# Kernel optimization log

Hardware: AMD Instinct MI355X
Metric: run time of the kernel (lower is better)

## Reference

```python
import jax, jax.numpy as jnp
import numpy as np

EMBED = 384; HEADS = 12; POINTS = 9; LAYERS = 2
KFG = 20; KBG = 50; NITER = 10
B = 4; H = 64; W = 64


def _layer_norm(x, g, b, eps=1e-5):
    m = x.mean(-1, keepdims=True)
    v = ((x - m) ** 2).mean(-1, keepdims=True)
    return (x - m) * jax.lax.rsqrt(v + eps) * g + b


def _sine_pos(pad, C):
    # pad [B,H,W], 1.0 = padded. SinePositionalEncoding(num_feats=C//2, normalize=True)
    nf = C // 2
    not_m = 1.0 - pad
    y = jnp.cumsum(not_m, axis=1)
    x = jnp.cumsum(not_m, axis=2)
    eps = 1e-6; sc = 2.0 * np.pi
    y = y / (y[:, -1:, :] + eps) * sc
    x = x / (x[:, :, -1:] + eps) * sc
    t = jnp.arange(nf, dtype=jnp.float32)
    dim_t = 10000.0 ** (2.0 * jnp.floor(t / 2.0) / nf)
    px = x[..., None] / dim_t
    py = y[..., None] / dim_t
    def inter(p):
        b_, h_, w_, _ = p.shape
        return jnp.stack((jnp.sin(p[..., 0::2]), jnp.cos(p[..., 1::2])), -1).reshape(b_, h_, w_, nf)
    pos = jnp.concatenate([inter(py), inter(px)], -1)  # [B,H,W,C]
    return pos.reshape(pad.shape[0], -1, C)


def _kmeans(x, w, K, n_iter):
    # masked Lloyd k-means. x [B,N,C], w [B,N] in {0,1} (1 = member of the group)
    Bq, N, C = x.shape
    score = w - (jnp.arange(N, dtype=x.dtype) / N) * 1e-3  # earliest in-group points first
    _, idx = jax.lax.top_k(score, K)
    centers = jnp.take_along_axis(x, idx[:, :, None], axis=1)  # [B,K,C]
    xsq = jnp.sum(x * x, -1)
    def body(i, c):
        d = xsq[:, :, None] - 2.0 * jnp.einsum('bnc,bkc->bnk', x, c) + jnp.sum(c * c, -1)[:, None, :]
        a = jax.nn.one_hot(jnp.argmin(d, -1), K, dtype=x.dtype) * w[:, :, None]
        num = jnp.einsum('bnk,bnc->bkc', a, x)
        den = jnp.sum(a, 1)[:, :, None]
        return jnp.where(den > 0, num / jnp.maximum(den, 1e-6), c)
    return jax.lax.fori_loop(0, n_iter, body, centers)


def _bilinear(value, loc, Hs, Ws):
    # value [B,heads,HW,hd]; loc [B,N,heads,P,2] normalized (x,y); zero padding outside
    Bq, nh, HW, hd = value.shape
    x = loc[..., 0] * Ws - 0.5
    y = loc[..., 1] * Hs - 0.5
    x0 = jnp.floor(x); y0 = jnp.floor(y)
    def tr(t):
        return jnp.transpose(t, (0, 2, 1, 3)).reshape(Bq, nh, -1)  # -> [B,heads,N*P]
    wx = tr(x - x0)[..., None]
    wy = tr(y - y0)[..., None]
    x0i = x0.astype(jnp.int32); y0i = y0.astype(jnp.int32)
    def gather(xi, yi):
        valid = (xi >= 0) & (xi < Ws) & (yi >= 0) & (yi < Hs)
        idx = jnp.clip(yi, 0, Hs - 1) * Ws + jnp.clip(xi, 0, Ws - 1)
        g = jnp.take_along_axis(value, tr(idx)[..., None], axis=2)  # [B,heads,N*P,hd]
        return g * tr(valid.astype(value.dtype))[..., None]
    v00 = gather(x0i, y0i)
    v01 = gather(x0i + 1, y0i)
    v10 = gather(x0i, y0i + 1)
    v11 = gather(x0i + 1, y0i + 1)
    out = v00 * (1 - wx) * (1 - wy) + v01 * wx * (1 - wy) + v10 * (1 - wx) * wy + v11 * wx * wy
    return out.reshape(Bq, nh, -1, POINTS, hd)  # [B,heads,N,P,hd]


def _forward(s_x, s_padding_mask, supp_mask, Wv, bv, Woff, boff, Wa, ba, Wout, bout,
             ln1_g, ln1_b, Wf1, Wf2, ln2_g, ln2_b):
    Bq, C, Hs, Ws = s_x.shape
    N = Hs * Ws
    hd = C // HEADS
    pad = (s_padding_mask[:, 0] == 255.0).astype(s_x.dtype)  # 1 = padded
    obj = (supp_mask[:, 0] == 1.0).astype(s_x.dtype)
    x = s_x.reshape(Bq, C, N).transpose(0, 2, 1)  # [B,N,C]
    padf = pad.reshape(Bq, N)
    objf = obj.reshape(Bq, N)
    # FG/BG k-means clustering of valid pixels (Cluster tool, n_iter=10)
    fg_c = _kmeans(x, objf * (1.0 - padf), KFG, NITER)
    bg_c = _kmeans(x, (1.0 - objf) * (1.0 - padf), KBG, NITER)
    pos = _sine_pos(pad, C)
    ry, rx = jnp.meshgrid(jnp.linspace(0.5, Hs - 0.5, Hs) / Hs,
                          jnp.linspace(0.5, Ws - 0.5, Ws) / Ws, indexing='ij')
    ref = jnp.stack([rx.reshape(-1), ry.reshape(-1)], -1)[None]  # [1,N,2] (x,y)
    wh = jnp.array([Ws, Hs], dtype=s_x.dtype)
    for l in range(LAYERS):
        q = x + pos
        v = (x * (1.0 - padf)[..., None]) @ Wv[l] + bv[l]
        v = v.reshape(Bq, N, HEADS, hd).transpose(0, 2, 1, 3)  # [B,heads,N,hd]
        off = (q @ Woff[l] + boff[l]).reshape(Bq, N, HEADS, POINTS, 2)
        aw = jax.nn.softmax((q @ Wa[l] + ba[l]).reshape(Bq, N, HEADS, POINTS), axis=-1)
        loc = ref[:, :, None, None, :] + off / wh
        samp = _bilinear(v, loc, Hs, Ws)  # [B,heads,N,P,hd]
        attn = jnp.einsum('bhnpd,bnhp->bnhd', samp, aw).reshape(Bq, N, C)
        x = _layer_norm(x + attn @ Wout[l] + bout[l], ln1_g[l], ln1_b[l])
        x = _layer_norm(x + jax.nn.relu(x @ Wf1[l]) @ Wf2[l], ln2_g[l], ln2_b[l])
    return jnp.concatenate([x, fg_c, bg_c], axis=1)  # [B, N+70, C]


def setup_inputs():
    key = jax.random.key(0)
    ks = jax.random.split(key, 12)
    dt = jnp.float32
    s = 0.02
    p = lambda k, shp: jax.random.normal(k, shp, dt) * s
    s_x = jax.random.normal(ks[0], (B, EMBED, H, W), dt)
    pad = jnp.zeros((B, 1, H, W), dt).at[:, :, :, W - 8:].set(255.0)  # right border padded
    supp_mask = (jax.random.uniform(ks[1], (B, 1, H, W)) < 0.15).astype(dt)
    return dict(
        s_x=s_x, s_padding_mask=pad, supp_mask=supp_mask,
        Wv=p(ks[2], (LAYERS, EMBED, EMBED)), bv=jnp.zeros((LAYERS, EMBED), dt),
        Woff=p(ks[3], (LAYERS, EMBED, HEADS * POINTS * 2)), boff=p(ks[4], (LAYERS, HEADS * POINTS * 2)),
        Wa=p(ks[5], (LAYERS, EMBED, HEADS * POINTS)), ba=jnp.zeros((LAYERS, HEADS * POINTS), dt),
        Wout=p(ks[6], (LAYERS, EMBED, EMBED)), bout=jnp.zeros((LAYERS, EMBED), dt),
        ln1_g=jnp.ones((LAYERS, EMBED), dt), ln1_b=jnp.zeros((LAYERS, EMBED), dt),
        Wf1=p(ks[7], (LAYERS, EMBED, 3 * EMBED)), Wf2=p(ks[8], (LAYERS, 3 * EMBED, EMBED)),
        ln2_g=jnp.ones((LAYERS, EMBED), dt), ln2_b=jnp.zeros((LAYERS, EMBED), dt))


def reference(s_x, s_padding_mask, supp_mask, Wv, bv, Woff, boff, Wa, ba, Wout, bout,
              ln1_g, ln1_b, Wf1, Wf2, ln2_g, ln2_b):
    return _forward(s_x, s_padding_mask, supp_mask, Wv, bv, Woff, boff, Wa, ba, Wout, bout,
                    ln1_g, ln1_b, Wf1, Wf2, ln2_g, ln2_b)
```

## Files before the change

kernel.cpp:

```cpp
#include <hip/hip_runtime.h>
#include <hip/hip_bf16.h>
#include <math.h>

#define NB 4
#define CE 384
#define NH 12
#define DH 32
#define NPTS 9
#define NLAYERS 2
#define KFG 20
#define KBG 50
#define NITER 10
#define HDIM 64
#define WDIM 64
#define NPIX 4096
#define BNTOT (NB * NPIX)
#define NROW (NPIX + KFG + KBG)
#define TWO_PI 6.283185307179586f

#define AS1 __attribute__((address_space(1)))
#define AS3 __attribute__((address_space(3)))

typedef __attribute__((ext_vector_type(8))) short short8;
typedef __attribute__((ext_vector_type(4))) float float4v;

static __device__ __forceinline__ unsigned short f2bf(float f) {
  __hip_bfloat16 h = __float2bfloat16(f);
  return *reinterpret_cast<unsigned short*>(&h);
}
static __device__ __forceinline__ float bf2f(unsigned short u) {
  unsigned x = ((unsigned)u) << 16;
  return __uint_as_float(x);
}

__device__ __forceinline__ float4 sample4(const float* __restrict__ vb, int xi, int yi, int c) {
  bool valid = (xi >= 0) & (xi < WDIM) & (yi >= 0) & (yi < HDIM);
  int xc = min(max(xi, 0), WDIM - 1), yc = min(max(yi, 0), HDIM - 1);
  float4 g = *(const float4*)(vb + (long)(yc * WDIM + xc) * CE + c);
  if (!valid) { g.x = 0.f; g.y = 0.f; g.z = 0.f; g.w = 0.f; }
  return g;
}

__global__ void k_masks(const float* __restrict__ pm, const float* __restrict__ sm,
                        float* padf, float* objf, float* notp, float* wfg, float* wbg) {
  int i = blockIdx.x * 256 + threadIdx.x;
  if (i >= NB * NPIX) return;
  float p  = (pm[i] == 255.0f) ? 1.f : 0.f;
  float o  = (sm[i] == 1.0f) ? 1.f : 0.f;
  float np_ = 1.f - p;
  padf[i] = p; objf[i] = o; notp[i] = np_;
  wfg[i] = o * np_;
  wbg[i] = (1.f - o) * np_;
}

__global__ __launch_bounds__(256) void k_transpose(const float* __restrict__ sx,
                                                   float* __restrict__ X) {
  __shared__ float tile[64][65];
  int nb = blockIdx.x * 64, cb = blockIdx.y * 64, b = blockIdx.z;
  int t = threadIdx.x;
  for (int idx = t; idx < 64 * 64; idx += 256) {
    int cc = idx >> 6, nn = idx & 63;
    tile[cc][nn] = sx[((long)b * CE + cb + cc) * NPIX + nb + nn];
  }
  __syncthreads();
  for (int idx = t; idx < 64 * 64; idx += 256) {
    int nn = idx >> 6, cc = idx & 63;
    X[((long)b * NPIX + nb + nn) * CE + cb + cc] = tile[cc][nn];
  }
}

__global__ void k_xsq(const float* __restrict__ X, double* __restrict__ xsq) {
  int row = blockIdx.x; int t = threadIdx.x;
  const float* xr = X + (long)row * CE;
  double s = 0.0;
  for (int i = t; i < CE; i += 64) { double v = (double)xr[i]; s += v * v; }
  #pragma unroll
  for (int o = 32; o > 0; o >>= 1) s += __shfl_down(s, o, 64);
  if (t == 0) xsq[row] = s;
}

__global__ __launch_bounds__(128) void k_cums(const float* __restrict__ padf,
                                              float* __restrict__ yvf,
                                              float* __restrict__ xvf,
                                              float* __restrict__ invdt) {
  __shared__ float pad_s[NPIX];
  int b = blockIdx.x; int t = threadIdx.x;
  for (int i = t; i < NPIX; i += 128) pad_s[i] = padf[b * NPIX + i];
  if (b == 0) {
    for (int c = t; c < CE; c += 128) {
      int tt = (c < 192) ? c : c - 192;
      invdt[c] = 1.0f / powf(10000.0f, (float)(2 * (tt / 2)) / 192.0f);
    }
  }
  __syncthreads();
  if (t < 64) {
    int w = t;
    float cum[64]; float tot = 0.f;
    for (int h = 0; h < 64; ++h) {
      float nm = 1.f - pad_s[h * WDIM + w];
      tot += nm; cum[h] = tot;
    }
    float sc = 1.f / (tot + 1e-6f);
    for (int h = 0; h < 64; ++h) yvf[b * NPIX + h * WDIM + w] = cum[h] * sc * TWO_PI;
  } else {
    int h = t - 64;
    float cum[64]; float tot = 0.f;
    for (int w = 0; w < 64; ++w) {
      float nm = 1.f - pad_s[h * WDIM + w];
      tot += nm; cum[w] = tot;
    }
    float sc = 1.f / (tot + 1e-6f);
    for (int w = 0; w < 64; ++w) xvf[b * NPIX + h * WDIM + w] = cum[w] * sc * TWO_PI;
  }
}

__global__ void k_kinit(const float* __restrict__ X, const float* __restrict__ wts,
                        double* __restrict__ cen, int K) {
  int b = blockIdx.x;
  __shared__ int idx[KBG];
  if (threadIdx.x == 0) {
    int cnt = 0;
    for (int n = 0; n < NPIX && cnt < K; ++n) if (wts[b * NPIX + n] > 0.f) idx[cnt++] = n;
    for (int n = 0; n < NPIX && cnt < K; ++n) if (!(wts[b * NPIX + n] > 0.f)) idx[cnt++] = n;
  }
  __syncthreads();
  for (int i = threadIdx.x; i < K * CE; i += blockDim.x) {
    int k = i / CE, c = i % CE;
    cen[((long)b * K + k) * CE + c] = (double)X[((long)b * NPIX + idx[k]) * CE + c];
  }
}

#define HSTR 98
#define KSTR 392

__global__ __launch_bounds__(1024) void k_dots(
    const float* __restrict__ X, const double* __restrict__ xsq,
    const double* __restrict__ cenF, const double* __restrict__ cenB,
    double* __restrict__ candD, int* __restrict__ candI, int* __restrict__ cntAll) {
  __shared__ double ct[10 * KSTR];
  __shared__ double csq_s[10];
  int z = blockIdx.y;
  int isBg = (z >= 2) ? 1 : 0;
  int k0 = isBg ? (z - 2) * 10 : z * 10;
  int t = threadIdx.x;
  int h = t & 3;
  int n = blockIdx.x * 256 + (t >> 2);
  int b = blockIdx.x >> 4;
  if (blockIdx.x == 0 && z == 0) {
    for (int i = t; i < NB * (KFG + KBG); i += 1024) cntAll[i] = 0;
  }
  const double* cb = (isBg ? cenB + (long)b * KBG * CE
                           : cenF + (long)b * KFG * CE) + (long)k0 * CE;
  for (int i = t; i < 10 * CE; i += 1024) {
    int k = i / CE, c = i % CE;
    ct[k * KSTR + (c / 96) * HSTR + (c % 96)] = cb[i];
  }
  if (t < 640) {
    int kk = t >> 6, lane = t & 63;
    double s = 0.0;
    for (int c = lane; c < CE; c += 64) { double v = cb[kk * CE + c]; s += v * v; }
    #pragma unroll
    for (int o = 32; o > 0; o >>= 1) s += __shfl_down(s, o, 64);
    if (lane == 0) csq_s[kk] = s;
  }
  __syncthreads();
  const float* xr = X + (long)n * CE + h * 96;
  const double* cth = ct + h * HSTR;
  double acc[10];
  #pragma unroll
  for (int k = 0; k < 10; ++k) acc[k] = 0.0;
  for (int c0 = 0; c0 < 96; c0 += 8) {
    double xd[8];
    float4 u = *(const float4*)(xr + c0);
    float4 v = *(const float4*)(xr + c0 + 4);
    xd[0] = u.x; xd[1] = u.y; xd[2] = u.z; xd[3] = u.w;
    xd[4] = v.x; xd[5] = v.y; xd[6] = v.z; xd[7] = v.w;
    #pragma unroll
    for (int k = 0; k < 10; ++k) {
      #pragma unroll
      for (int j = 0; j < 8; j += 2) {
        double2 cv = *(const double2*)(&cth[k * KSTR + c0 + j]);
        acc[k] += xd[j] * cv.x;
        acc[k] += xd[j + 1] * cv.y;
      }
    }
  }
  #pragma unroll
  for (int k = 0; k < 10; ++k) {
    double a = acc[k];
    a += __shfl_xor(a, 1, 64);
    a += __shfl_xor(a, 2, 64);
    acc[k] = a;
  }
  if (h == 0) {
    double q = xsq[n];
    double best = 1.0e300; int bi = 0;
    #pragma unroll
    for (int k = 0; k < 10; ++k) {
      double d = q - 2.0 * acc[k] + csq_s[k];
      if (d < best) { best = d; bi = k0 + k; }
    }
    long gi = (long)z * BNTOT + n;
    candD[gi] = best;
    candI[gi] = bi;
  }
}

__global__ void k_asn(const double* __restrict__ candD, const int* __restrict__ candI,
                      const float* __restrict__ wfg, const float* __restrict__ wbg,
                      int* __restrict__ listF, int* __restrict__ listB,
                      int* __restrict__ cntAll) {
  int n = blockIdx.x * 256 + threadIdx.x;
  if (n >= BNTOT) return;
  int b = n >> 12;
  int nn = n & (NPIX - 1);
  float wf = wfg[n], wb = wbg[n];
  if (wf > 0.f) {
    double d0 = candD[n]; int i0 = candI[n];
    double d1 = candD[(long)BNTOT + n];
    if (d1 < d0) { d0 = d1; i0 = candI[(long)BNTOT + n]; }
    int slot = atomicAdd(&cntAll[b * KFG + i0], 1);
    listF[((long)b * KFG + i0) * NPIX + slot] = nn;
  } else if (wb > 0.f) {
    double d0 = candD[2L * BNTOT + n]; int i0 = candI[2L * BNTOT + n];
    #pragma unroll
    for (int z = 3; z < 7; ++z) {
      double dz = candD[(long)z * BNTOT + n];
      if (dz < d0) { d0 = dz; i0 = candI[(long)z * BNTOT + n]; }
    }
    int slot = atomicAdd(&cntAll[NB * KFG + b * KBG + i0], 1);
    listB[((long)b * KBG + i0) * NPIX + slot] = nn;
  }
}

__global__ __launch_bounds__(128) void k_cacc(
    const float* __restrict__ X,
    const int* __restrict__ listF, const int* __restrict__ listB,
    const int* __restrict__ cntAll,
    const double* __restrict__ srcF, double* __restrict__ dstF,
    const double* __restrict__ srcB, double* __restrict__ dstB) {
  __shared__ int ls[NPIX];
  int slice = blockIdx.x;
  int kq = blockIdx.y;
  int b = blockIdx.z;
  int t = threadIdx.x;
  int c = slice * 128 + t;
  const int* list; int cnt; const double* src; double* dst; long o;
  if (kq < KFG) {
    cnt = cntAll[b * KFG + kq];
    list = listF + ((long)b * KFG + kq) * NPIX;
    o = ((long)b * KFG + kq) * CE + c;
    src = srcF; dst = dstF;
  } else {
    int k = kq - KFG;
    cnt = cntAll[NB * KFG + b * KBG + k];
    list = listB + ((long)b * KBG + k) * NPIX;
    o = ((long)b * KBG + k) * CE + c;
    src = srcB; dst = dstB;
  }
  for (int i = t; i < cnt; i += 128) ls[i] = list[i];
  __syncthreads();
  const float* Xb = X + (long)b * NPIX * CE;
  double acc = 0.0;
  int i = 0;
  for (; i + 4 <= cnt; i += 4) {
    int n0 = ls[i], n1 = ls[i + 1], n2 = ls[i + 2], n3 = ls[i + 3];
    float v0 = Xb[(long)n0 * CE + c];
    float v1 = Xb[(long)n1 * CE + c];
    float v2 = Xb[(long)n2 * CE + c];
    float v3 = Xb[(long)n3 * CE + c];
    acc += (double)v0; acc += (double)v1; acc += (double)v2; acc += (double)v3;
  }
  for (; i < cnt; ++i) acc += (double)Xb[(long)ls[i] * CE + c];
  dst[o] = (cnt > 0) ? (acc / (double)cnt) : src[o];
}

__global__ void k_cvtQV(const float* __restrict__ X,
                        const float* __restrict__ yvf, const float* __restrict__ xvf,
                        const float* __restrict__ invdt, const float* __restrict__ notp,
                        float* __restrict__ POS,
                        unsigned short* __restrict__ QB, unsigned short* __restrict__ VBin) {
  long i = (long)blockIdx.x * 256 + threadIdx.x;
  if (i >= (long)NB * NPIX * CE) return;
  int c = (int)(i % CE);
  long row = i / CE;
  float p = (c < 192) ? yvf[row] : xvf[row];
  float v = p * invdt[c];
  int tt = (c < 192) ? c : c - 192;
  float r = (tt & 1) ? cosf(v) : sinf(v);
  POS[i] = r;
  float x = X[i];
  QB[i] = f2bf(x + r);
  VBin[i] = f2bf(x * notp[row]);
}

__global__ void k_cvtW_all(
    const float* __restrict__ Wv_l, const float* __restrict__ Woff_l,
    const float* __restrict__ Wa_l, const float* __restrict__ Wout_l,
    const float* __restrict__ Wf1_l, const float* __restrict__ Wf2_l,
    const float* __restrict__ boff_l, const float* __restrict__ ba_l,
    unsigned short* __restrict__ W0, unsigned short* __restrict__ W1,
    unsigned short* __restrict__ W3, unsigned short* __restrict__ W4,
    unsigned short* __restrict__ W5, float* __restrict__ biasCat) {
  int i = blockIdx.x * 256 + threadIdx.x;
  const int S = 147456, SF = 442368;
  if (i < S) {
    int n = i / 384, k = i % 384;
    W0[i] = f2bf(Wv_l[(long)k * 384 + n]);
  } else if (i < 2 * S) {
    int j = i - S; int n = j / 384, k = j % 384;
    float v = 0.f;
    if (n < 216) v = Woff_l[(long)k * 216 + n];
    else if (n < 324) v = Wa_l[(long)k * 108 + (n - 216)];
    W1[j] = f2bf(v);
  } else if (i < 3 * S) {
    int j = i - 2 * S; int n = j / 384, k = j % 384;
    W3[j] = f2bf(Wout_l[(long)k * 384 + n]);
  } else if (i < 3 * S + SF) {
    int j = i - 3 * S; int n = j / 384, k = j % 384;
    W4[j] = f2bf(Wf1_l[(long)k * 1152 + n]);
  } else if (i < 3 * S + 2 * SF) {
    int j = i - 3 * S - SF; int n = j / 1152, k = j % 1152;
    W5[j] = f2bf(Wf2_l[(long)k * 384 + n]);
  } else if (i < 3 * S + 2 * SF + 324) {
    int j = i - 3 * S - 2 * SF;
    biasCat[j] = (j < 216) ? boff_l[j] : ba_l[j - 216];
  }
}

__global__ __launch_bounds__(256) void k_gemm_bf(
    const unsigned short* __restrict__ A, const unsigned short* __restrict__ Bt,
    const float* __restrict__ bias, float* __restrict__ Cf, unsigned short* __restrict__ Cb,
    int M, int K, int N, int relu) {
  __shared__ unsigned short As[128 * 32];
  __shared__ unsigned short Bs[128 * 32];
  int m0 = blockIdx.y * 128, n0 = blockIdx.x * 128;
  int t = threadIdx.x;
  int w = t >> 6, l = t & 63;
  int wm = w >> 1, wn = w & 1;
  int half = l >> 4, lr = l & 15;
  float4v acc[4][4] = {};
  for (int k0 = 0; k0 < K; k0 += 32) {
    #pragma unroll
    for (int i = 0; i < 2; ++i) {
      int c = w * 64 + i * 256 + l;
      int r = c >> 2, part = c & 3;
      int ldsOff = (w * 64 + i * 256) * 8;
      __builtin_amdgcn_global_load_lds(
          (const AS1 unsigned int*)(A + (size_t)(m0 + r) * K + k0 + part * 8),
          (AS3 unsigned int*)(As + ldsOff), 16, 0, 0);
      __builtin_amdgcn_global_load_lds(
          (const AS1 unsigned int*)(Bt + (size_t)(n0 + r) * K + k0 + part * 8),
          (AS3 unsigned int*)(Bs + ldsOff), 16, 0, 0);
    }
    __syncthreads();
    short8 af[4], bfr[4];
    #pragma unroll
    for (int am = 0; am < 4; ++am)
      af[am] = *(const short8*)(&As[(wm * 64 + am * 16 + lr) * 32 + half * 8]);
    #pragma unroll
    for (int bn = 0; bn < 4; ++bn)
      bfr[bn] = *(const short8*)(&Bs[(wn * 64 + bn * 16 + lr) * 32 + half * 8]);
    #pragma unroll
    for (int am = 0; am < 4; ++am)
      #pragma unroll
      for (int bn = 0; bn < 4; ++bn)
        acc[am][bn] = __builtin_amdgcn_mfma_f32_16x16x32_bf16(af[am], bfr[bn], acc[am][bn], 0, 0, 0);
    __syncthreads();
  }
  #pragma unroll
  for (int am = 0; am < 4; ++am) {
    #pragma unroll
    for (int bn = 0; bn < 4; ++bn) {
      int gc = n0 + wn * 64 + bn * 16 + lr;
      if (gc < N) {
        float bv = bias ? bias[gc] : 0.f;
        int gr0 = m0 + wm * 64 + am * 16 + half * 4;
        #pragma unroll
        for (int r = 0; r < 4; ++r) {
          float v = acc[am][bn][r] + bv;
          if (relu) v = fmaxf(v, 0.f);
          size_t oi = (size_t)(gr0 + r) * N + gc;
          if (Cf) Cf[oi] = v;
          else Cb[oi] = f2bf(v);
        }
      }
    }
  }
}

__global__ void k_coords(const unsigned short* __restrict__ OAB, float4* __restrict__ CRD) {
  int idx = blockIdx.x * 256 + threadIdx.x;
  if (idx >= NB * NPIX * NH) return;
  int row = idx / NH, h = idx % NH;
  int n = row & (NPIX - 1);
  int hh = n >> 6, ww = n & 63;
  float refx = ((float)ww + 0.5f) / (float)WDIM;
  float refy = ((float)hh + 0.5f) / (float)HDIM;
  const unsigned short* oab = OAB + (size_t)row * 324;
  float f[NPTS];
  #pragma unroll
  for (int j = 0; j < NPTS; ++j) f[j] = bf2f(oab[216 + h * 9 + j]);
  float m = f[0];
  #pragma unroll
  for (int j = 1; j < NPTS; ++j) m = fmaxf(m, f[j]);
  float s = 0.f;
  #pragma unroll
  for (int j = 0; j < NPTS; ++j) { f[j] = expf(f[j] - m); s += f[j]; }
  float inv = 1.f / s;
  float4* crd = CRD + (size_t)row * 108 + h * 9;
  #pragma unroll
  for (int p = 0; p < NPTS; ++p) {
    float ox = bf2f(oab[h * 18 + p * 2 + 0]);
    float oy = bf2f(oab[h * 18 + p * 2 + 1]);
    float lx = refx + ox / (float)WDIM;
    float ly = refy + oy / (float)HDIM;
    float xs = lx * (float)WDIM - 0.5f;
    float ys = ly * (float)HDIM - 0.5f;
    float x0f = floorf(xs), y0f = floorf(ys);
    int x0 = (int)x0f, y0 = (int)y0f;
    float4 o;
    o.x = xs - x0f;
    o.y = ys - y0f;
    o.z = f[p] * inv;
    o.w = __int_as_float((y0 << 16) | (x0 & 0xFFFF));
    crd[p] = o;
  }
}

__global__ __launch_bounds__(256) void k_gather(
    const float* __restrict__ V, const float4* __restrict__ CRD,
    uint2* __restrict__ ATTu) {
  int idx = blockIdx.x * 256 + threadIdx.x;
  if (idx >= NB * NPIX * (CE / 4)) return;
  int row = idx / (CE / 4), cq = idx % (CE / 4);
  int c = cq * 4;
  int h = c >> 5;
  int b = row >> 12;
  const float* vb = V + (size_t)b * NPIX * CE;
  const float4* crd = CRD + (size_t)row * 108 + h * 9;
  float a0 = 0.f, a1 = 0.f, a2 = 0.f, a3 = 0.f;
  #pragma unroll
  for (int p = 0; p < NPTS; ++p) {
    float4 o = crd[p];
    int pk = __float_as_int(o.w);
    int x0 = (int)(short)(pk & 0xFFFF);
    int y0 = pk >> 16;
    float wx = o.x, wy = o.y, aw = o.z;
    float4 g00 = sample4(vb, x0,     y0,     c);
    float4 g01 = sample4(vb, x0 + 1, y0,     c);
    float4 g10 = sample4(vb, x0,     y0 + 1, c);
    float4 g11 = sample4(vb, x0 + 1, y0 + 1, c);
    float w00 = (1.f - wx) * (1.f - wy), w01 = wx * (1.f - wy);
    float w10 = (1.f - wx) * wy,         w11 = wx * wy;
    a0 += aw * (g00.x * w00 + g01.x * w01 + g10.x * w10 + g11.x * w11);
    a1 += aw * (g00.y * w00 + g01.y * w01 + g10.y * w10 + g11.y * w11);
    a2 += aw * (g00.z * w00 + g01.z * w01 + g10.z * w10 + g11.z * w11);
    a3 += aw * (g00.w * w00 + g01.w * w01 + g10.w * w10 + g11.w * w11);
  }
  uint2 pk2;
  pk2.x = (unsigned)f2bf(a0) | ((unsigned)f2bf(a1) << 16);
  pk2.y = (unsigned)f2bf(a2) | ((unsigned)f2bf(a3) << 16);
  ATTu[(size_t)row * (CE / 4) + cq] = pk2;
}

__global__ __launch_bounds__(256) void k_ln(
    float* __restrict__ X, const float* __restrict__ T,
    const float* __restrict__ g, const float* __restrict__ bb,
    unsigned short* __restrict__ xbOut,
    const float* __restrict__ posp, const float* __restrict__ notp,
    unsigned short* __restrict__ qb, unsigned short* __restrict__ vbin,
    float* __restrict__ outp) {
  int t = threadIdx.x;
  int row = blockIdx.x * 4 + (t >> 6);
  int lane = t & 63;
  float* xr = X + (long)row * CE;
  const float* tr = T + (long)row * CE;
  float v[6]; float s = 0.f;
  #pragma unroll
  for (int i = 0; i < 6; ++i) { v[i] = xr[lane + 64 * i] + tr[lane + 64 * i]; s += v[i]; }
  #pragma unroll
  for (int o = 32; o > 0; o >>= 1) s += __shfl_down(s, o, 64);
  s = __shfl(s, 0, 64);
  float m = s / (float)CE;
  float var = 0.f;
  #pragma unroll
  for (int i = 0; i < 6; ++i) { float d = v[i] - m; var += d * d; }
  #pragma unroll
  for (int o = 32; o > 0; o >>= 1) var += __shfl_down(var, o, 64);
  var = __shfl(var, 0, 64);
  float rst = rsqrtf(var / (float)CE + 1e-5f);
  float nprow = notp ? notp[row] : 0.f;
  int b = row >> 12, n = row & (NPIX - 1);
  #pragma unroll
  for (int i = 0; i < 6; ++i) {
    int c = lane + 64 * i;
    float xn = (v[i] - m) * rst * g[c] + bb[c];
    if (outp) outp[((long)b * NROW + n) * CE + c] = xn;
    else xr[c] = xn;
    if (xbOut) xbOut[(long)row * CE + c] = f2bf(xn);
    if (qb) {
      qb[(long)row * CE + c] = f2bf(xn + posp[(long)row * CE + c]);
      vbin[(long)row * CE + c] = f2bf(xn * nprow);
    }
  }
}

__global__ void k_out_cen(const double* __restrict__ fg, const double* __restrict__ bg,
                          float* __restrict__ out) {
  int i = blockIdx.x * 256 + threadIdx.x;
  const int tot = NB * (KFG + KBG) * CE;
  if (i >= tot) return;
  int c = i % CE;
  int r = i / CE;
  int rr = r % (KFG + KBG);
  int b = r / (KFG + KBG);
  float v;
  if (rr < KFG) v = (float)fg[((long)b * KFG + rr) * CE + c];
  else v = (float)bg[((long)b * KBG + (rr - KFG)) * CE + c];
  out[((long)b * NROW + NPIX + rr) * CE + c] = v;
}

extern "C" void kernel_launch(void* const* d_in, const int* in_sizes, int n_in,
                              void* d_out, int out_size, void* d_ws, size_t ws_size,
                              hipStream_t stream) {
  (void)in_sizes; (void)n_in; (void)out_size; (void)ws_size;
  const float* s_x  = (const float*)d_in[0];
  const float* s_pm = (const float*)d_in[1];
  const float* s_sm = (const float*)d_in[2];
  const float* Wv   = (const float*)d_in[3];
  const float* bv   = (const float*)d_in[4];
  const float* Woff = (const float*)d_in[5];
  const float* boff = (const float*)d_in[6];
  const float* Wa   = (const float*)d_in[7];
  const float* ba   = (const float*)d_in[8];
  const float* Wout = (const float*)d_in[9];
  const float* bout = (const float*)d_in[10];
  const float* ln1g = (const float*)d_in[11];
  const float* ln1b = (const float*)d_in[12];
  const float* Wf1  = (const float*)d_in[13];
  const float* Wf2  = (const float*)d_in[14];
  const float* ln2g = (const float*)d_in[15];
  const float* ln2b = (const float*)d_in[16];
  float* out = (float*)d_out;
  char* pb = (char*)d_ws;

  const long BN  = (long)NB * NPIX;
  const long BNC = BN * CE;

  float* X    = (float*)pb; pb += BNC * 4;
  float* POS  = (float*)pb; pb += BNC * 4;
  float* V    = (float*)pb; pb += BNC * 4;
  float* T2   = (float*)pb; pb += BNC * 4;
  unsigned short* QB   = (unsigned short*)pb; pb += BNC * 2;
  unsigned short* VBin = (unsigned short*)pb; pb += BNC * 2;
  unsigned short* T1b  = (unsigned short*)pb; pb += BNC * 2;
  unsigned short* Zbf  = QB;
  unsigned short* XB   = (unsigned short*)pb; pb += BNC * 2;
  unsigned short* OAB  = (unsigned short*)pb; pb += BN * 324 * 2;
  float4* CRD = (float4*)pb; pb += BN * 108 * 16;
  const int S_W = 147456, S_F = 442368;
  unsigned short* WT[NLAYERS][5];
  float* biasCat[NLAYERS];
  for (int l = 0; l < NLAYERS; ++l) {
    WT[l][0] = (unsigned short*)pb; pb += S_W * 2;
    WT[l][1] = (unsigned short*)pb; pb += S_W * 2;
    WT[l][2] = (unsigned short*)pb; pb += S_W * 2;
    WT[l][3] = (unsigned short*)pb; pb += S_F * 2;
    WT[l][4] = (unsigned short*)pb; pb += S_F * 2;
    biasCat[l] = (float*)pb; pb += 324 * 4;
  }
  float* padf = (float*)pb; pb += BN * 4;
  float* objf = (float*)pb; pb += BN * 4;
  float* notp = (float*)pb; pb += BN * 4;
  float* wfg  = (float*)pb; pb += BN * 4;
  float* wbg  = (float*)pb; pb += BN * 4;
  float* yvf  = (float*)pb; pb += BN * 4;
  float* xvf  = (float*)pb; pb += BN * 4;
  float* invdt = (float*)pb; pb += CE * 4;
  pb = (char*)(((size_t)pb + 7) & ~(size_t)7);
  double* xsq   = (double*)pb; pb += BN * 8;
  double* candD = (double*)pb; pb += BN * 7 * 8;
  double* cFgA = (double*)pb; pb += (long)NB * KFG * CE * 8;
  double* cFgB = (double*)pb; pb += (long)NB * KFG * CE * 8;
  double* cBgA = (double*)pb; pb += (long)NB * KBG * CE * 8;
  double* cBgB = (double*)pb; pb += (long)NB * KBG * CE * 8;
  int* candI  = (int*)pb; pb += BN * 7 * 4;
  int* cntAll = (int*)pb; pb += NB * (KFG + KBG) * 4;
  int* listF  = (int*)pb; pb += (long)NB * KFG * NPIX * 4;
  int* listB  = (int*)pb; pb += (long)NB * KBG * NPIX * 4;

  int bn = (int)BN;
  int cvtBlocks = (int)((BNC + 255) / 256);

  k_masks<<<(bn + 255) / 256, 256, 0, stream>>>(s_pm, s_sm, padf, objf, notp, wfg, wbg);
  k_transpose<<<dim3(NPIX / 64, CE / 64, NB), 256, 0, stream>>>(s_x, X);
  k_xsq<<<bn, 64, 0, stream>>>(X, xsq);
  k_cums<<<NB, 128, 0, stream>>>(padf, yvf, xvf, invdt);
  k_cvtQV<<<cvtBlocks, 256, 0, stream>>>(X, yvf, xvf, invdt, notp, POS, QB, VBin);

  const int CVTW_TOT = 3 * S_W + 2 * S_F + 324;
  for (int l = 0; l < NLAYERS; ++l) {
    k_cvtW_all<<<(CVTW_TOT + 255) / 256, 256, 0, stream>>>(
        Wv + (long)l * CE * CE, Woff + (long)l * CE * 216, Wa + (long)l * CE * 108,
        Wout + (long)l * CE * CE, Wf1 + (long)l * CE * 1152, Wf2 + (long)l * 1152 * CE,
        boff + l * 216, ba + l * 108,
        WT[l][0], WT[l][1], WT[l][2], WT[l][3], WT[l][4], biasCat[l]);
  }

  double *srcF = cFgA, *dstF = cFgB, *srcB = cBgA, *dstB = cBgB;
  k_kinit<<<NB, 256, 0, stream>>>(X, wfg, srcF, KFG);
  k_kinit<<<NB, 256, 0, stream>>>(X, wbg, srcB, KBG);
  for (int it = 0; it < NITER; ++it) {
    k_dots<<<dim3(bn / 256, 7), 1024, 0, stream>>>(X, xsq, srcF, srcB, candD, candI, cntAll);
    k_asn<<<(bn + 255) / 256, 256, 0, stream>>>(candD, candI, wfg, wbg, listF, listB, cntAll);
    k_cacc<<<dim3(3, KFG + KBG, NB), 128, 0, stream>>>(
        X, listF, listB, cntAll, srcF, dstF, srcB, dstB);
    double* tmp;
    tmp = srcF; srcF = dstF; dstF = tmp;
    tmp = srcB; srcB = dstB; dstB = tmp;
  }
  double* fgC = srcF; double* bgC = srcB;

  for (int l = 0; l < NLAYERS; ++l) {
    const float* bv_l   = bv   + l * CE;
    const float* bout_l = bout + l * CE;
    int last = (l == NLAYERS - 1);

    k_gemm_bf<<<dim3(3, 128), 256, 0, stream>>>(VBin, WT[l][0], bv_l, V, (unsigned short*)nullptr,
                                                bn, CE, 384, 0);
    k_gemm_bf<<<dim3(3, 128), 256, 0, stream>>>(QB, WT[l][1], biasCat[l], (float*)nullptr, OAB,
                                                bn, CE, 324, 0);
    k_coords<<<(bn * NH + 255) / 256, 256, 0, stream>>>(OAB, CRD);
    k_gather<<<(bn * (CE / 4) + 255) / 256, 256, 0, stream>>>(V, CRD, (uint2*)T1b);
    k_gemm_bf<<<dim3(3, 128), 256, 0, stream>>>(T1b, WT[l][2], bout_l, T2, (unsigned short*)nullptr,
                                                bn, CE, 384, 0);
    k_ln<<<bn / 4, 256, 0, stream>>>(X, T2, ln1g + l * CE, ln1b + l * CE,
                                     XB, (const float*)nullptr, (const float*)nullptr,
                                     (unsigned short*)nullptr, (unsigned short*)nullptr,
                                     (float*)nullptr);
    k_gemm_bf<<<dim3(9, 128), 256, 0, stream>>>(XB, WT[l][3], (const float*)nullptr,
                                                (float*)nullptr, Zbf, bn, CE, 1152, 1);
    k_gemm_bf<<<dim3(3, 128), 256, 0, stream>>>(Zbf, WT[l][4], (const float*)nullptr,
                                                T2, (unsigned short*)nullptr, bn, 1152, 384, 0);
    if (!last) {
      k_ln<<<bn / 4, 256, 0, stream>>>(X, T2, ln2g + l * CE, ln2b + l * CE,
                                       (unsigned short*)nullptr, POS, notp, QB, VBin,
                                       (float*)nullptr);
    } else {
      k_ln<<<bn / 4, 256, 0, stream>>>(X, T2, ln2g + l * CE, ln2b + l * CE,
                                       (unsigned short*)nullptr, (const float*)nullptr,
                                       (const float*)nullptr, (unsigned short*)nullptr,
                                       (unsigned short*)nullptr, out);
    }
  }

  k_out_cen<<<(NB * (KFG + KBG) * CE + 255) / 256, 256, 0, stream>>>(fgC, bgC, out);
}
```

Measured before the change: 1.477 ms.

## Register-block k-means distance kernel over 4 points and remap GEMM blocks by XCD

The k-means distance kernel now runs 256 threads per block, and each 4-thread group handles 4 points instead of 1. Each centroid value read from shared memory is therefore reused across 4 points in registers, which cuts LDS traffic per FMA and amortizes the centroid staging and sum-of-squares work over more points per block. The cost is more accumulator registers (40 doubles) and strided global loads of X across 4 rows. Separately, the bf16 GEMM remaps block indices so that consecutive blocks dispatched to the same XCD cover neighbouring M tiles, aiming at better L2 locality.

```diff
diff --git a/kernel.cpp b/kernel.cpp
--- a/kernel.cpp
+++ b/kernel.cpp
@@ -133,7 +133,7 @@
 #define HSTR 98
 #define KSTR 392
 
-__global__ __launch_bounds__(1024) void k_dots(
+__global__ __launch_bounds__(256, 4) void k_dots(
     const float* __restrict__ X, const double* __restrict__ xsq,
     const double* __restrict__ cenF, const double* __restrict__ cenB,
     double* __restrict__ candD, int* __restrict__ candI, int* __restrict__ cntAll) {
@@ -144,65 +144,75 @@
   int k0 = isBg ? (z - 2) * 10 : z * 10;
   int t = threadIdx.x;
   int h = t & 3;
-  int n = blockIdx.x * 256 + (t >> 2);
+  int n = blockIdx.x * 256 + (t >> 2) * 4;
   int b = blockIdx.x >> 4;
   if (blockIdx.x == 0 && z == 0) {
-    for (int i = t; i < NB * (KFG + KBG); i += 1024) cntAll[i] = 0;
+    for (int i = t; i < NB * (KFG + KBG); i += 256) cntAll[i] = 0;
   }
   const double* cb = (isBg ? cenB + (long)b * KBG * CE
                            : cenF + (long)b * KFG * CE) + (long)k0 * CE;
-  for (int i = t; i < 10 * CE; i += 1024) {
+  for (int i = t; i < 10 * CE; i += 256) {
     int k = i / CE, c = i % CE;
     ct[k * KSTR + (c / 96) * HSTR + (c % 96)] = cb[i];
   }
-  if (t < 640) {
-    int kk = t >> 6, lane = t & 63;
-    double s = 0.0;
-    for (int c = lane; c < CE; c += 64) { double v = cb[kk * CE + c]; s += v * v; }
-    #pragma unroll
-    for (int o = 32; o > 0; o >>= 1) s += __shfl_down(s, o, 64);
-    if (lane == 0) csq_s[kk] = s;
+  {
+    int w = t >> 6, lane = t & 63;
+    for (int kk = w; kk < 10; kk += 4) {
+      double s = 0.0;
+      for (int c = lane; c < CE; c += 64) { double v = cb[kk * CE + c]; s += v * v; }
+      #pragma unroll
+      for (int o = 32; o > 0; o >>= 1) s += __shfl_down(s, o, 64);
+      if (lane == 0) csq_s[kk] = s;
+    }
   }
   __syncthreads();
   const float* xr = X + (long)n * CE + h * 96;
   const double* cth = ct + h * HSTR;
-  double acc[10];
-  #pragma unroll
-  for (int k = 0; k < 10; ++k) acc[k] = 0.0;
-  for (int c0 = 0; c0 < 96; c0 += 8) {
-    double xd[8];
-    float4 u = *(const float4*)(xr + c0);
-    float4 v = *(const float4*)(xr + c0 + 4);
-    xd[0] = u.x; xd[1] = u.y; xd[2] = u.z; xd[3] = u.w;
-    xd[4] = v.x; xd[5] = v.y; xd[6] = v.z; xd[7] = v.w;
+  double acc[10][4];
+  #pragma unroll
+  for (int k = 0; k < 10; ++k)
+    #pragma unroll
+    for (int p = 0; p < 4; ++p) acc[k][p] = 0.0;
+  for (int c0 = 0; c0 < 96; c0 += 2) {
+    double xd[4][2];
+    #pragma unroll
+    for (int p = 0; p < 4; ++p) {
+      float2 f = *(const float2*)(xr + p * CE + c0);
+      xd[p][0] = (double)f.x; xd[p][1] = (double)f.y;
+    }
     #pragma unroll
     for (int k = 0; k < 10; ++k) {
+      double2 cv = *(const double2*)(&cth[k * KSTR + c0]);
       #pragma unroll
-      for (int j = 0; j < 8; j += 2) {
-        double2 cv = *(const double2*)(&cth[k * KSTR + c0 + j]);
-        acc[k] += xd[j] * cv.x;
-        acc[k] += xd[j + 1] * cv.y;
+      for (int p = 0; p < 4; ++p) {
+        acc[k][p] += xd[p][0] * cv.x;
+        acc[k][p] += xd[p][1] * cv.y;
       }
     }
   }
   #pragma unroll
-  for (int k = 0; k < 10; ++k) {
-    double a = acc[k];
-    a += __shfl_xor(a, 1, 64);
-    a += __shfl_xor(a, 2, 64);
-    acc[k] = a;
-  }
+  for (int k = 0; k < 10; ++k)
+    #pragma unroll
+    for (int p = 0; p < 4; ++p) {
+      double a = acc[k][p];
+      a += __shfl_xor(a, 1, 64);
+      a += __shfl_xor(a, 2, 64);
+      acc[k][p] = a;
+    }
   if (h == 0) {
-    double q = xsq[n];
-    double best = 1.0e300; int bi = 0;
-    #pragma unroll
-    for (int k = 0; k < 10; ++k) {
-      double d = q - 2.0 * acc[k] + csq_s[k];
-      if (d < best) { best = d; bi = k0 + k; }
-    }
-    long gi = (long)z * BNTOT + n;
-    candD[gi] = best;
-    candI[gi] = bi;
+    #pragma unroll
+    for (int p = 0; p < 4; ++p) {
+      double qn = xsq[n + p];
+      double best = 1.0e300; int bi = 0;
+      #pragma unroll
+      for (int k = 0; k < 10; ++k) {
+        double d = qn - 2.0 * acc[k][p] + csq_s[k];
+        if (d < best) { best = d; bi = k0 + k; }
+      }
+      long gi = (long)z * BNTOT + n + p;
+      candD[gi] = best;
+      candI[gi] = bi;
+    }
   }
 }
 
@@ -334,7 +344,18 @@
     int M, int K, int N, int relu) {
   __shared__ unsigned short As[128 * 32];
   __shared__ unsigned short Bs[128 * 32];
-  int m0 = blockIdx.y * 128, n0 = blockIdx.x * 128;
+  int bx, by;
+  {
+    int gx = gridDim.x;
+    int q = blockIdx.y * gx + blockIdx.x;
+    if ((gridDim.y & 7) == 0) {
+      int xcd = q & 7;
+      int r = q >> 3;
+      bx = r % gx;
+      by = xcd + 8 * (r / gx);
+    } else { bx = blockIdx.x; by = blockIdx.y; }
+  }
+  int m0 = by * 128, n0 = bx * 128;
   int t = threadIdx.x;
   int w = t >> 6, l = t & 63;
   int wm = w >> 1, wn = w & 1;
@@ -612,7 +633,7 @@
   k_kinit<<<NB, 256, 0, stream>>>(X, wfg, srcF, KFG);
   k_kinit<<<NB, 256, 0, stream>>>(X, wbg, srcB, KBG);
   for (int it = 0; it < NITER; ++it) {
-    k_dots<<<dim3(bn / 256, 7), 1024, 0, stream>>>(X, xsq, srcF, srcB, candD, candI, cntAll);
+    k_dots<<<dim3(bn / 256, 7), 256, 0, stream>>>(X, xsq, srcF, srcB, candD, candI, cntAll);
     k_asn<<<(bn + 255) / 256, 256, 0, stream>>>(candD, candI, wfg, wbg, listF, listB, cntAll);
     k_cacc<<<dim3(3, KFG + KBG, NB), 128, 0, stream>>>(
         X, listF, listB, cntAll, srcF, dstF, srcB, dstB);
```

After: 2.262 ms. 1.53x slower.
